# Optimization experiments

Measured on AMD Instinct MI355X. Metric: run time of the kernel, lower is better.

The kernel has to match this reference:

```python
import jax, jax.numpy as jnp
import numpy as np

N_EMBED = 1024
N_HEAD = 16
HEAD_DIM = N_EMBED // N_HEAD


def setup_inputs() -> dict:
    key = jax.random.key(0)
    ks = jax.random.split(key, 6)
    B, T, C = 4, 2048, N_EMBED
    scale = 1.0 / np.sqrt(C)
    x = jax.random.normal(ks[0], (B, T, C), dtype=jnp.float32)
    # torch nn.Linear weights are [out, in]; y = x @ W.T
    Wk = jax.random.normal(ks[1], (C, C), dtype=jnp.float32) * scale
    Wq = jax.random.normal(ks[2], (C, C), dtype=jnp.float32) * scale
    Wv = jax.random.normal(ks[3], (C, C), dtype=jnp.float32) * scale
    Wp = jax.random.normal(ks[4], (C, C), dtype=jnp.float32) * scale
    bp = jax.random.normal(ks[5], (C,), dtype=jnp.float32) * 0.01
    return {"x": x, "Wk": Wk, "Wq": Wq, "Wv": Wv, "Wp": Wp, "bp": bp}


def reference(x, Wk, Wq, Wv, Wp, bp):
    B, T, C = x.shape
    H, D = N_HEAD, HEAD_DIM
    # QKV projections (torch Linear: x @ W.T), split heads -> [B, H, T, D]
    k = (x @ Wk.T).reshape(B, T, H, D).transpose(0, 2, 1, 3)
    q = (x @ Wq.T).reshape(B, T, H, D).transpose(0, 2, 1, 3)
    v = (x @ Wv.T).reshape(B, T, H, D).transpose(0, 2, 1, 3)
    # scaled scores [B, H, T, T]
    att = jnp.einsum('bhtd,bhsd->bhts', q, k) * (1.0 / np.sqrt(D))
    causal = jnp.tril(jnp.ones((T, T), dtype=bool))
    att = jnp.where(causal[None, None, :, :], att, -jnp.inf)
    att = jax.nn.softmax(att, axis=-1)
    out = jnp.einsum('bhts,bhsd->bhtd', att, v)  # [B, H, T, D]
    out = out.transpose(0, 2, 1, 3).reshape(B, T, C)
    out = out @ Wp.T + bp
    return out
```

## Files before the change

kernel.cpp:

```cpp
#include <hip/hip_runtime.h>

typedef __bf16 bf16_t;
typedef bf16_t bf16x4 __attribute__((ext_vector_type(4)));
typedef bf16_t bf16x8 __attribute__((ext_vector_type(8)));
typedef float f32x4 __attribute__((ext_vector_type(4)));

#define B_ 4
#define T_ 2048
#define C_ 1024
#define H_ 16
#define D_ 64

#define GLDS(g, l)                                                          \
  __builtin_amdgcn_global_load_lds(                                         \
      (const __attribute__((address_space(1))) void*)(g),                   \
      (__attribute__((address_space(3))) void*)(l), 16, 0, 0)

static __device__ __forceinline__ f32x4 mfma16(bf16x8 a, bf16x8 b, f32x4 c) {
  return __builtin_amdgcn_mfma_f32_16x16x32_bf16(a, b, c, 0, 0, 0);
}

static __device__ __forceinline__ float exp2_hw(float x) {
  float r;
  asm("v_exp_f32 %0, %1" : "=v"(r) : "v"(x));
  return r;
}

__global__ void cvt_all(const float* __restrict__ x, const float* __restrict__ wq,
                        const float* __restrict__ wk, const float* __restrict__ wv,
                        const float* __restrict__ wp, bf16_t* __restrict__ xb,
                        bf16_t* __restrict__ wqb, bf16_t* __restrict__ wkb,
                        bf16_t* __restrict__ wvb, bf16_t* __restrict__ wpb) {
  int i = blockIdx.x * blockDim.x + threadIdx.x;
  const float* src;
  bf16_t* dst;
  int off;
  if (i < 2097152) {
    src = x; dst = xb; off = i;
  } else {
    int r = i - 2097152;
    int region = r >> 18;
    off = r & 262143;
    if (region == 0) { src = wq; dst = wqb; }
    else if (region == 1) { src = wk; dst = wkb; }
    else if (region == 2) { src = wv; dst = wvb; }
    else { src = wp; dst = wpb; }
  }
  float4 v = ((const float4*)src)[off];
  bf16x4 o = {(bf16_t)v.x, (bf16_t)v.y, (bf16_t)v.z, (bf16_t)v.w};
  ((bf16x4*)dst)[off] = o;
}

__global__ __launch_bounds__(512) void gemm_qkv(
    const bf16_t* __restrict__ xb, const bf16_t* __restrict__ wq,
    const bf16_t* __restrict__ wk, const bf16_t* __restrict__ wv,
    bf16_t* __restrict__ qo, bf16_t* __restrict__ ko, bf16_t* __restrict__ vt) {
  __shared__ bf16_t lA[2][128 * 64];
  __shared__ bf16_t lB[2][3][128 * 64];
  const int tid = threadIdx.x, wave = tid >> 6, lane = tid & 63;
  const int g = lane >> 4;
  const int bid = blockIdx.x;
  const int swz = ((bid & 7) << 6) | (bid >> 3);
  const int col0 = (swz & 7) * 128, row0 = (swz >> 3) * 128;
  const int wr = wave >> 2, wc = wave & 3;
  f32x4 acc[3][4][2] = {};

  const int soff[2] = {wave * 1024, (8 + wave) * 1024};
  size_t sgo[2];
#pragma unroll
  for (int i = 0; i < 2; ++i) {
    const int lin = soff[i] + lane * 16;
    const int r = lin >> 7;
    const int c = ((lin >> 4) & 7) ^ (r & 7);
    sgo[i] = (size_t)r * C_ + c * 8;
  }

#define QKV_STAGE(k0, b)                                                    \
  {                                                                         \
    _Pragma("unroll") for (int i = 0; i < 2; ++i) {                         \
      GLDS(xb + (size_t)row0 * C_ + (k0) + sgo[i], &lA[b][soff[i] >> 1]);   \
      GLDS(wq + (size_t)col0 * C_ + (k0) + sgo[i], &lB[b][0][soff[i] >> 1]);\
      GLDS(wk + (size_t)col0 * C_ + (k0) + sgo[i], &lB[b][1][soff[i] >> 1]);\
      GLDS(wv + (size_t)col0 * C_ + (k0) + sgo[i], &lB[b][2][soff[i] >> 1]);\
    }                                                                       \
  }

  QKV_STAGE(0, 0);
  int cur = 0;
  for (int k0 = 0; k0 < C_; k0 += 64) {
    __syncthreads();
    if (k0 + 64 < C_) QKV_STAGE(k0 + 64, cur ^ 1);
#pragma unroll
    for (int s = 0; s < 2; ++s) {
      const int c = s * 4 + g;
      bf16x8 af[4];
#pragma unroll
      for (int m = 0; m < 4; ++m) {
        const int r = wr * 64 + m * 16 + (lane & 15);
        af[m] = *(const bf16x8*)((const char*)lA[cur] + r * 128 +
                                 ((c ^ (r & 7)) << 4));
      }
#pragma unroll
      for (int z = 0; z < 3; ++z) {
        bf16x8 bfr[2];
#pragma unroll
        for (int n = 0; n < 2; ++n) {
          const int r = wc * 32 + n * 16 + (lane & 15);
          bfr[n] = *(const bf16x8*)((const char*)lB[cur][z] + r * 128 +
                                    ((c ^ (r & 7)) << 4));
        }
#pragma unroll
        for (int m = 0; m < 4; ++m)
#pragma unroll
          for (int n = 0; n < 2; ++n)
            acc[z][m][n] = mfma16(af[m], bfr[n], acc[z][m][n]);
      }
    }
    cur ^= 1;
  }
#pragma unroll
  for (int z = 0; z < 3; ++z) {
    bf16_t* outb = (z == 0) ? qo : ((z == 1) ? ko : vt);
    const float qs = (z == 0) ? 0.125f * 1.4426950408889634f : 1.0f;
#pragma unroll
    for (int m = 0; m < 4; ++m) {
#pragma unroll
      for (int n = 0; n < 2; ++n) {
        const int gr = row0 + wr * 64 + m * 16 + ((lane >> 4) << 2);
        const int gc = col0 + wc * 32 + n * 16 + (lane & 15);
        const int b = gr >> 11, t = gr & (T_ - 1);
        const int h = gc >> 6, d = gc & 63;
        if (z < 2) {
#pragma unroll
          for (int j = 0; j < 4; ++j)
            outb[(((size_t)(b * H_ + h)) * T_ + (t + j)) * D_ + d] =
                (bf16_t)(acc[z][m][n][j] * qs);
        } else {
          bf16x4 pk = {(bf16_t)acc[z][m][n][0], (bf16_t)acc[z][m][n][1],
                       (bf16_t)acc[z][m][n][2], (bf16_t)acc[z][m][n][3]};
          *(bf16x4*)(outb + (((size_t)(b * H_ + h)) * D_ + d) * T_ + t) = pk;
        }
      }
    }
  }
}

__global__ __launch_bounds__(256) void gemm_proj(const bf16_t* __restrict__ att,
                                                 const bf16_t* __restrict__ wp,
                                                 const float* __restrict__ bias,
                                                 float* __restrict__ out) {
  __shared__ bf16_t lA[2][128 * 64];
  __shared__ bf16_t lB[2][128 * 64];
  const int tid = threadIdx.x;
  const int wave = tid >> 6, lane = tid & 63;
  const int wr = wave >> 1, wc = wave & 1;
  const int row0 = blockIdx.y * 128, col0 = blockIdx.x * 128;
  f32x4 acc[4][4] = {};

  const int soff[4] = {wave * 1024, (4 + wave) * 1024, (8 + wave) * 1024,
                       (12 + wave) * 1024};
  size_t sgo[4];
#pragma unroll
  for (int i = 0; i < 4; ++i) {
    const int lin = soff[i] + lane * 16;
    const int r = lin >> 7;
    const int c = ((lin >> 4) & 7) ^ (r & 7);
    sgo[i] = (size_t)r * C_ + c * 8;
  }

#define PROJ_STAGE(k0, b)                                                   \
  {                                                                         \
    _Pragma("unroll") for (int i = 0; i < 4; ++i) {                         \
      GLDS(att + (size_t)row0 * C_ + (k0) + sgo[i], &lA[b][soff[i] >> 1]);  \
      GLDS(wp + (size_t)col0 * C_ + (k0) + sgo[i], &lB[b][soff[i] >> 1]);   \
    }                                                                       \
  }

  PROJ_STAGE(0, 0);
  int cur = 0;
  for (int k0 = 0; k0 < C_; k0 += 64) {
    __syncthreads();
    if (k0 + 64 < C_) PROJ_STAGE(k0 + 64, cur ^ 1);
#pragma unroll
    for (int s = 0; s < 2; ++s) {
      bf16x8 af[4], bfr[4];
#pragma unroll
      for (int m = 0; m < 4; ++m) {
        const int r = wr * 64 + m * 16 + (lane & 15);
        const int c = s * 4 + (lane >> 4);
        af[m] = *(const bf16x8*)((const char*)lA[cur] + r * 128 +
                                 ((c ^ (r & 7)) << 4));
      }
#pragma unroll
      for (int n = 0; n < 4; ++n) {
        const int r = wc * 64 + n * 16 + (lane & 15);
        const int c = s * 4 + (lane >> 4);
        bfr[n] = *(const bf16x8*)((const char*)lB[cur] + r * 128 +
                                  ((c ^ (r & 7)) << 4));
      }
#pragma unroll
      for (int m = 0; m < 4; ++m)
#pragma unroll
        for (int n = 0; n < 4; ++n) acc[m][n] = mfma16(af[m], bfr[n], acc[m][n]);
    }
    cur ^= 1;
  }
#pragma unroll
  for (int m = 0; m < 4; ++m) {
#pragma unroll
    for (int n = 0; n < 4; ++n) {
      const int gr = row0 + wr * 64 + m * 16 + ((lane >> 4) << 2);
      const int gc = col0 + wc * 64 + n * 16 + (lane & 15);
      const float bv = bias[gc];
#pragma unroll
      for (int j = 0; j < 4; ++j)
        out[(size_t)(gr + j) * C_ + gc] = acc[m][n][j] + bv;
    }
  }
}

__global__ __launch_bounds__(512, 4) void attn_fwd(
    const bf16_t* __restrict__ Q, const bf16_t* __restrict__ K,
    const bf16_t* __restrict__ V, bf16_t* __restrict__ AO) {
  __shared__ bf16_t lK[2][2][64 * 64];
  __shared__ bf16_t lV[2][2][64 * 64];
  __shared__ bf16_t lP[8][16 * 64];
  const int tid = threadIdx.x, wave = tid >> 6, lane = tid & 63;
  const int g = lane >> 4;
  const int bh = blockIdx.y;
  const size_t baseK = (size_t)bh * T_ * D_;
  const size_t baseV = (size_t)bh * D_ * T_;
  const int bb = bh >> 4, hh = bh & 15;

  int koff[2][4];
#pragma unroll
  for (int s = 0; s < 2; ++s)
#pragma unroll
    for (int nf = 0; nf < 4; ++nf) {
      const int r = nf * 16 + (lane & 15);
      const int c = s * 4 + g;
      koff[s][nf] = r * 128 + ((c ^ (r & 7)) << 4);
    }
  int pwoff[4];
  {
    const int r = lane & 15;
#pragma unroll
    for (int nf = 0; nf < 4; ++nf)
      pwoff[nf] = r * 128 + (((2 * nf + (g >> 1)) ^ (r & 7)) << 4) +
                  ((g & 1) << 3);
  }
  const int soff = wave * 1024;
  const int slin = soff + lane * 16;
  const int srow = slin >> 7;
  const int scol = ((slin >> 4) & 7) ^ (srow & 7);
  const size_t kgo = (size_t)srow * D_ + scol * 8;
  const size_t vgo = (size_t)srow * T_ + scol * 8;

  for (int half = 0; half < 2; ++half) {
    const int qt = half ? (15 - blockIdx.x) : blockIdx.x;
    const int twv = qt * 128 + wave * 16;
    const int ntiles = qt + 1;
    __syncthreads();
#pragma unroll
    for (int sub = 0; sub < 2; ++sub) {
      GLDS(K + baseK + (size_t)sub * 64 * D_ + kgo, &lK[0][sub][soff >> 1]);
      GLDS(V + baseV + (size_t)sub * 64 + vgo, &lV[0][sub][soff >> 1]);
    }
    bf16x8 qf[2];
#pragma unroll
    for (int s = 0; s < 2; ++s)
      qf[s] = *(const bf16x8*)(Q + baseK +
                               (size_t)(twv + (lane & 15)) * D_ + s * 32 +
                               (g << 3));
    float lrun = 0.f;
    f32x4 o[4] = {};
    int cur = 0;
    for (int it = 0; it < ntiles; ++it) {
      __syncthreads();
      if (it + 1 < ntiles) {
        const int nb = cur ^ 1;
        const size_t ks = (size_t)(it + 1) * 128;
#pragma unroll
        for (int sub = 0; sub < 2; ++sub) {
          GLDS(K + baseK + (ks + sub * 64) * D_ + kgo,
               &lK[nb][sub][soff >> 1]);
          GLDS(V + baseV + ks + sub * 64 + vgo, &lV[nb][sub][soff >> 1]);
        }
      }
      const int s0 = it * 128;
      f32x4 sc[2][4];
#pragma unroll
      for (int sub = 0; sub < 2; ++sub)
#pragma unroll
        for (int nf = 0; nf < 4; ++nf) sc[sub][nf] = (f32x4){};
      __builtin_amdgcn_s_setprio(1);
#pragma unroll
      for (int sub = 0; sub < 2; ++sub) {
        const char* kb = (const char*)lK[cur][sub];
#pragma unroll
        for (int s = 0; s < 2; ++s)
#pragma unroll
          for (int nf = 0; nf < 4; ++nf)
            sc[sub][nf] =
                mfma16(*(const bf16x8*)(kb + koff[s][nf]), qf[s], sc[sub][nf]);
      }
      __builtin_amdgcn_s_setprio(0);
      if (it == qt) {
        const int t = twv + (lane & 15);
#pragma unroll
        for (int sub = 0; sub < 2; ++sub)
#pragma unroll
          for (int nf = 0; nf < 4; ++nf)
#pragma unroll
            for (int j = 0; j < 4; ++j) {
              const int s = s0 + sub * 64 + nf * 16 + g * 4 + j;
              if (s > t) sc[sub][nf][j] = -1e30f;
            }
      }
      float ps = 0.f;
      bf16x4 pk[2][4];
#pragma unroll
      for (int sub = 0; sub < 2; ++sub) {
        float psn[4];
#pragma unroll
        for (int nf = 0; nf < 4; ++nf) {
          float e0 = exp2_hw(sc[sub][nf][0]);
          float e1 = exp2_hw(sc[sub][nf][1]);
          float e2 = exp2_hw(sc[sub][nf][2]);
          float e3 = exp2_hw(sc[sub][nf][3]);
          pk[sub][nf][0] = (bf16_t)e0;
          pk[sub][nf][1] = (bf16_t)e1;
          pk[sub][nf][2] = (bf16_t)e2;
          pk[sub][nf][3] = (bf16_t)e3;
          psn[nf] = (e0 + e1) + (e2 + e3);
        }
        ps += (psn[0] + psn[1]) + (psn[2] + psn[3]);
      }
      ps += __shfl_xor(ps, 16);
      ps += __shfl_xor(ps, 32);
      lrun += ps;
      __builtin_amdgcn_s_setprio(1);
#pragma unroll
      for (int sub = 0; sub < 2; ++sub) {
        char* pw = (char*)lP[wave];
#pragma unroll
        for (int nf = 0; nf < 4; ++nf) *(bf16x4*)(pw + pwoff[nf]) = pk[sub][nf];
        const char* pb = (const char*)lP[wave];
        const char* vb = (const char*)lV[cur][sub];
#pragma unroll
        for (int s2 = 0; s2 < 2; ++s2) {
          bf16x8 pf = *(const bf16x8*)(pb + koff[s2][0]);
#pragma unroll
          for (int df = 0; df < 4; ++df)
            o[df] = mfma16(pf, *(const bf16x8*)(vb + koff[s2][df]), o[df]);
        }
      }
      __builtin_amdgcn_s_setprio(0);
      cur ^= 1;
    }
    {
      const float inv = 1.0f / lrun;
      float ib[4];
#pragma unroll
      for (int j = 0; j < 4; ++j)
        ib[j] = __shfl(inv, (lane & 48) | ((g << 2) + j));
#pragma unroll
      for (int j = 0; j < 4; ++j) {
        const int t = twv + (g << 2) + j;
#pragma unroll
        for (int df = 0; df < 4; ++df) {
          const int cc = hh * 64 + df * 16 + (lane & 15);
          AO[((size_t)(bb * T_ + t)) * C_ + cc] = (bf16_t)(o[df][j] * ib[j]);
        }
      }
    }
  }
}

extern "C" void kernel_launch(void* const* d_in, const int* in_sizes, int n_in,
                              void* d_out, int out_size, void* d_ws,
                              size_t ws_size, hipStream_t stream) {
  const float* x = (const float*)d_in[0];
  const float* Wk = (const float*)d_in[1];
  const float* Wq = (const float*)d_in[2];
  const float* Wv = (const float*)d_in[3];
  const float* Wp = (const float*)d_in[4];
  const float* bp = (const float*)d_in[5];
  char* ws = (char*)d_ws;
  bf16_t* xb = (bf16_t*)ws;
  bf16_t* wqb = (bf16_t*)(ws + (16u << 20));
  bf16_t* wkb = (bf16_t*)(ws + (18u << 20));
  bf16_t* wvb = (bf16_t*)(ws + (20u << 20));
  bf16_t* wpb = (bf16_t*)(ws + (22u << 20));
  bf16_t* q = (bf16_t*)(ws + (24u << 20));
  bf16_t* k = (bf16_t*)(ws + (40u << 20));
  bf16_t* vt = (bf16_t*)(ws + (56u << 20));
  bf16_t* att = xb;

  cvt_all<<<12288, 256, 0, stream>>>(x, Wq, Wk, Wv, Wp, xb, wqb, wkb, wvb, wpb);
  gemm_qkv<<<512, 512, 0, stream>>>(xb, wqb, wkb, wvb, q, k, vt);
  attn_fwd<<<dim3(8, 64), 512, 0, stream>>>(q, k, vt, att);
  gemm_proj<<<dim3(8, 64), 256, 0, stream>>>(att, wpb, bp, (float*)d_out);
}
```

Baseline: 162.7 us.

## Halve QKV GEMM column tile to 64, doubling blocks and raising occupancy

The fused QKV projection GEMM now uses 128x64 output tiles per matrix instead of 128x128, launching 1024 blocks instead of 512. Each wave now holds 12 accumulator tiles instead of 24, which lowers register pressure, and the kernel requests four blocks per CU through launch bounds. The LDS offsets for the swizzled reads are computed once before the k loop. In exchange, the activation tile is reloaded twice as often, so less of it is reused per block and global/LDS traffic per FLOP rises.

```diff
diff --git a/kernel.cpp b/kernel.cpp
--- a/kernel.cpp
+++ b/kernel.cpp
@@ -51,38 +51,57 @@
   ((bf16x4*)dst)[off] = o;
 }
 
-__global__ __launch_bounds__(512) void gemm_qkv(
+__global__ __launch_bounds__(512, 4) void gemm_qkv(
     const bf16_t* __restrict__ xb, const bf16_t* __restrict__ wq,
     const bf16_t* __restrict__ wk, const bf16_t* __restrict__ wv,
     bf16_t* __restrict__ qo, bf16_t* __restrict__ ko, bf16_t* __restrict__ vt) {
   __shared__ bf16_t lA[2][128 * 64];
-  __shared__ bf16_t lB[2][3][128 * 64];
+  __shared__ bf16_t lB[2][3][64 * 64];
   const int tid = threadIdx.x, wave = tid >> 6, lane = tid & 63;
   const int g = lane >> 4;
   const int bid = blockIdx.x;
-  const int swz = ((bid & 7) << 6) | (bid >> 3);
-  const int col0 = (swz & 7) * 128, row0 = (swz >> 3) * 128;
+  const int swz = ((bid & 7) << 7) | (bid >> 3);
+  const int col0 = (swz & 15) * 64, row0 = (swz >> 4) * 128;
   const int wr = wave >> 2, wc = wave & 3;
-  f32x4 acc[3][4][2] = {};
-
-  const int soff[2] = {wave * 1024, (8 + wave) * 1024};
-  size_t sgo[2];
+  f32x4 acc[3][4] = {};
+
+  const int soffA[2] = {wave * 1024, (8 + wave) * 1024};
+  size_t sgoA[2];
 #pragma unroll
   for (int i = 0; i < 2; ++i) {
-    const int lin = soff[i] + lane * 16;
+    const int lin = soffA[i] + lane * 16;
     const int r = lin >> 7;
     const int c = ((lin >> 4) & 7) ^ (r & 7);
-    sgo[i] = (size_t)r * C_ + c * 8;
+    sgoA[i] = (size_t)r * C_ + c * 8;
+  }
+  const int soffB = wave * 1024;
+  size_t sgoB;
+  {
+    const int lin = soffB + lane * 16;
+    const int r = lin >> 7;
+    const int c = ((lin >> 4) & 7) ^ (r & 7);
+    sgoB = (size_t)r * C_ + c * 8;
+  }
+  int koffA[2][4], koffB[2];
+#pragma unroll
+  for (int s = 0; s < 2; ++s) {
+    const int c = s * 4 + g;
+#pragma unroll
+    for (int m = 0; m < 4; ++m) {
+      const int r = wr * 64 + m * 16 + (lane & 15);
+      koffA[s][m] = r * 128 + ((c ^ (r & 7)) << 4);
+    }
+    const int rb = wc * 16 + (lane & 15);
+    koffB[s] = rb * 128 + ((c ^ (rb & 7)) << 4);
   }
 
 #define QKV_STAGE(k0, b)                                                    \
   {                                                                         \
-    _Pragma("unroll") for (int i = 0; i < 2; ++i) {                         \
-      GLDS(xb + (size_t)row0 * C_ + (k0) + sgo[i], &lA[b][soff[i] >> 1]);   \
-      GLDS(wq + (size_t)col0 * C_ + (k0) + sgo[i], &lB[b][0][soff[i] >> 1]);\
-      GLDS(wk + (size_t)col0 * C_ + (k0) + sgo[i], &lB[b][1][soff[i] >> 1]);\
-      GLDS(wv + (size_t)col0 * C_ + (k0) + sgo[i], &lB[b][2][soff[i] >> 1]);\
-    }                                                                       \
+    GLDS(xb + (size_t)row0 * C_ + (k0) + sgoA[0], &lA[b][soffA[0] >> 1]);   \
+    GLDS(xb + (size_t)row0 * C_ + (k0) + sgoA[1], &lA[b][soffA[1] >> 1]);   \
+    GLDS(wq + (size_t)col0 * C_ + (k0) + sgoB, &lB[b][0][soffB >> 1]);      \
+    GLDS(wk + (size_t)col0 * C_ + (k0) + sgoB, &lB[b][1][soffB >> 1]);      \
+    GLDS(wv + (size_t)col0 * C_ + (k0) + sgoB, &lB[b][2][soffB >> 1]);      \
   }
 
   QKV_STAGE(0, 0);
@@ -92,28 +111,15 @@
     if (k0 + 64 < C_) QKV_STAGE(k0 + 64, cur ^ 1);
 #pragma unroll
     for (int s = 0; s < 2; ++s) {
-      const int c = s * 4 + g;
+      const char* ab = (const char*)lA[cur];
       bf16x8 af[4];
 #pragma unroll
-      for (int m = 0; m < 4; ++m) {
-        const int r = wr * 64 + m * 16 + (lane & 15);
-        af[m] = *(const bf16x8*)((const char*)lA[cur] + r * 128 +
-                                 ((c ^ (r & 7)) << 4));
-      }
+      for (int m = 0; m < 4; ++m) af[m] = *(const bf16x8*)(ab + koffA[s][m]);
 #pragma unroll
       for (int z = 0; z < 3; ++z) {
-        bf16x8 bfr[2];
-#pragma unroll
-        for (int n = 0; n < 2; ++n) {
-          const int r = wc * 32 + n * 16 + (lane & 15);
-          bfr[n] = *(const bf16x8*)((const char*)lB[cur][z] + r * 128 +
-                                    ((c ^ (r & 7)) << 4));
-        }
-#pragma unroll
-        for (int m = 0; m < 4; ++m)
-#pragma unroll
-          for (int n = 0; n < 2; ++n)
-            acc[z][m][n] = mfma16(af[m], bfr[n], acc[z][m][n]);
+        bf16x8 bf = *(const bf16x8*)((const char*)lB[cur][z] + koffB[s]);
+#pragma unroll
+        for (int m = 0; m < 4; ++m) acc[z][m] = mfma16(af[m], bf, acc[z][m]);
       }
     }
     cur ^= 1;
@@ -122,24 +128,21 @@
   for (int z = 0; z < 3; ++z) {
     bf16_t* outb = (z == 0) ? qo : ((z == 1) ? ko : vt);
     const float qs = (z == 0) ? 0.125f * 1.4426950408889634f : 1.0f;
+    const int gc = col0 + wc * 16 + (lane & 15);
+    const int h = gc >> 6, d = gc & 63;
 #pragma unroll
     for (int m = 0; m < 4; ++m) {
-#pragma unroll
-      for (int n = 0; n < 2; ++n) {
-        const int gr = row0 + wr * 64 + m * 16 + ((lane >> 4) << 2);
-        const int gc = col0 + wc * 32 + n * 16 + (lane & 15);
-        const int b = gr >> 11, t = gr & (T_ - 1);
-        const int h = gc >> 6, d = gc & 63;
-        if (z < 2) {
-#pragma unroll
-          for (int j = 0; j < 4; ++j)
-            outb[(((size_t)(b * H_ + h)) * T_ + (t + j)) * D_ + d] =
-                (bf16_t)(acc[z][m][n][j] * qs);
-        } else {
-          bf16x4 pk = {(bf16_t)acc[z][m][n][0], (bf16_t)acc[z][m][n][1],
-                       (bf16_t)acc[z][m][n][2], (bf16_t)acc[z][m][n][3]};
-          *(bf16x4*)(outb + (((size_t)(b * H_ + h)) * D_ + d) * T_ + t) = pk;
-        }
+      const int gr = row0 + wr * 64 + m * 16 + ((lane >> 4) << 2);
+      const int b = gr >> 11, t = gr & (T_ - 1);
+      if (z < 2) {
+#pragma unroll
+        for (int j = 0; j < 4; ++j)
+          outb[(((size_t)(b * H_ + h)) * T_ + (t + j)) * D_ + d] =
+              (bf16_t)(acc[z][m][j] * qs);
+      } else {
+        bf16x4 pk = {(bf16_t)acc[z][m][0], (bf16_t)acc[z][m][1],
+                     (bf16_t)acc[z][m][2], (bf16_t)acc[z][m][3]};
+        *(bf16x4*)(outb + (((size_t)(b * H_ + h)) * D_ + d) * T_ + t) = pk;
       }
     }
   }
@@ -398,7 +401,7 @@
   bf16_t* att = xb;
 
   cvt_all<<<12288, 256, 0, stream>>>(x, Wq, Wk, Wv, Wp, xb, wqb, wkb, wvb, wpb);
-  gemm_qkv<<<512, 512, 0, stream>>>(xb, wqb, wkb, wvb, q, k, vt);
+  gemm_qkv<<<1024, 512, 0, stream>>>(xb, wqb, wkb, wvb, q, k, vt);
   attn_fwd<<<dim3(8, 64), 512, 0, stream>>>(q, k, vt, att);
   gemm_proj<<<dim3(8, 64), 256, 0, stream>>>(att, wpb, bp, (float*)d_out);
 }
```

Measured after the change: 160.5 us. Within noise of the previous version (-1.4%).
